# Kernel optimization log

Measured on AMD Instinct MI355X. Metric: run time of the kernel, lower is better.

The kernel has to match this reference:

```python
import jax, jax.numpy as jnp
import numpy as np

N = 100000
E = 1600000
IN_C = 64
HID_C = 64
OUT_C = 64
GW = 0.8
EPS = 1e-5


def setup_inputs() -> dict:
    key = jax.random.key(0)
    ks = jax.random.split(key, 8)
    node_features = jax.random.normal(ks[0], (N, IN_C), dtype=jnp.float32)
    edges = jax.random.randint(ks[1], (2, E), 0, N, dtype=jnp.int64)
    s1 = 1.0 / np.sqrt(IN_C)
    s2 = 1.0 / np.sqrt(HID_C)
    W1 = jax.random.uniform(ks[2], (IN_C, HID_C), jnp.float32, -s1, s1)
    b1 = jnp.zeros((HID_C,), jnp.float32)
    W2 = jax.random.uniform(ks[3], (HID_C, OUT_C), jnp.float32, -s2, s2)
    b2 = jnp.zeros((OUT_C,), jnp.float32)
    ln_w = jnp.ones((1,), jnp.float32)
    ln_b = jnp.zeros((1,), jnp.float32)
    return {"node_features": node_features, "edges": edges, "W1": W1, "b1": b1,
            "W2": W2, "b2": b2, "ln_w": ln_w, "ln_b": ln_b}


def _gcn_conv(x, W, b, src, dst, enorm, n):
    # GCNConv: D^{-1/2}(A+I)D^{-1/2} X W + b  (self-loops already in src/dst)
    xw = x @ W                              # [N, F]
    msg = xw[src] * enorm[:, None]          # gather + scale, [E+N, F]
    out = jax.ops.segment_sum(msg, dst, num_segments=n)
    return out + b


def reference(node_features, edges, W1, b1, W2, b2, ln_w, ln_b):
    n = node_features.shape[0]
    loops = jnp.arange(n, dtype=edges.dtype)
    src = jnp.concatenate([edges[0], loops])
    dst = jnp.concatenate([edges[1], loops])
    deg = jax.ops.segment_sum(jnp.ones_like(dst, dtype=node_features.dtype), dst, num_segments=n)
    dis = jnp.where(deg > 0, jax.lax.rsqrt(deg), 0.0)
    enorm = dis[src] * dis[dst]

    # both branches apply the same conv1 to the same input (dropout off in eval)
    h = jax.nn.relu(_gcn_conv(node_features, W1, b1, src, dst, enorm, n))
    x = GW * h + (1.0 - GW) * h
    x = jax.nn.relu(_gcn_conv(x, W2, b2, src, dst, enorm, n))
    # PyG LayerNorm, mode='graph', batch=None: normalize over all nodes+channels
    mean = jnp.mean(x)
    var = jnp.mean((x - mean) ** 2)
    x = (x - mean) * jax.lax.rsqrt(var + EPS) * ln_w + ln_b
    return x
```

## Files before the change

### kernel.cpp

```cpp
#include <hip/hip_runtime.h>
#include <hip/hip_bf16.h>

#define CH 64
#define BSH 9
#define CHUNK 16384
#define MAXB 10240


__global__ __launch_bounds__(1024)
void coarse_hist_kernel(const int* __restrict__ dst, int* __restrict__ blockHist,
                        int E, int nb) {
    __shared__ int h[256];
    int t = threadIdx.x;
    for (int i = t; i < nb; i += 1024) h[i] = 0;
    __syncthreads();
    int base = blockIdx.x * CHUNK + t * 16;
#pragma unroll
    for (int j = 0; j < 16; j += 4) {
        int e = base + j;
        if (e + 3 < E) {
            int4 d = *(const int4*)(dst + e);
            atomicAdd(&h[d.x >> BSH], 1);
            atomicAdd(&h[d.y >> BSH], 1);
            atomicAdd(&h[d.z >> BSH], 1);
            atomicAdd(&h[d.w >> BSH], 1);
        } else {
            for (int k = e; k < E && k < e + 4; ++k) atomicAdd(&h[dst[k] >> BSH], 1);
        }
    }
    __syncthreads();
    for (int i = t; i < nb; i += 1024) blockHist[blockIdx.x * nb + i] = h[i];
}

__global__ __launch_bounds__(256)
void scan_hist_kernel(int* __restrict__ blockHist, int* __restrict__ bucketStart,
                      int nblk, int nb) {
    __shared__ int tots[256];
    __shared__ int scn[257];
    int t = threadIdx.x;
    if (t < nb) {
        int s = 0;
        for (int blk = 0; blk < nblk; ++blk) s += blockHist[blk * nb + t];
        tots[t] = s;
    }
    __syncthreads();
    if (t == 0) {
        int r = 0;
        for (int b = 0; b < nb; ++b) { scn[b] = r; r += tots[b]; }
        scn[nb] = r;
    }
    __syncthreads();
    if (t < nb) {
        int r = scn[t];
        for (int blk = 0; blk < nblk; ++blk) {
            int v = blockHist[blk * nb + t];
            blockHist[blk * nb + t] = r;
            r += v;
        }
    }
    if (t <= nb) bucketStart[t] = scn[t];
}

__global__ __launch_bounds__(1024)
void scatter_pairs_kernel(const int* __restrict__ src, const int* __restrict__ dst,
                          const int* __restrict__ blockBase, unsigned* __restrict__ pairs,
                          int E, int nb) {
    __shared__ int cur[256];
    int t = threadIdx.x;
    for (int i = t; i < nb; i += 1024) cur[i] = blockBase[blockIdx.x * nb + i];
    __syncthreads();
    int base = blockIdx.x * CHUNK + t * 16;
#pragma unroll
    for (int j = 0; j < 16; j += 4) {
        int e = base + j;
        if (e + 3 < E) {
            int4 d = *(const int4*)(dst + e);
            int4 s = *(const int4*)(src + e);
            int p0 = atomicAdd(&cur[d.x >> BSH], 1);
            pairs[p0] = ((unsigned)(d.x & 511) << 17) | (unsigned)s.x;
            int p1 = atomicAdd(&cur[d.y >> BSH], 1);
            pairs[p1] = ((unsigned)(d.y & 511) << 17) | (unsigned)s.y;
            int p2 = atomicAdd(&cur[d.z >> BSH], 1);
            pairs[p2] = ((unsigned)(d.z & 511) << 17) | (unsigned)s.z;
            int p3 = atomicAdd(&cur[d.w >> BSH], 1);
            pairs[p3] = ((unsigned)(d.w & 511) << 17) | (unsigned)s.w;
        } else {
            for (int k = e; k < E && k < e + 4; ++k) {
                int d = dst[k];
                int p = atomicAdd(&cur[d >> BSH], 1);
                pairs[p] = ((unsigned)(d & 511) << 17) | (unsigned)src[k];
            }
        }
    }
}

__global__ __launch_bounds__(1024)
void bucket_csr_kernel(const unsigned* __restrict__ pairs, const int* __restrict__ bucketStart,
                       int* __restrict__ col, int* __restrict__ rs, float* __restrict__ dis,
                       int N, int nb) {
    __shared__ int hist[512];
    __shared__ int offs[512];
    __shared__ int cursor[512];
    __shared__ int lcol[MAXB];
    int b = blockIdx.x;
    int t = threadIdx.x;
    int n0 = b << BSH;
    int nn = min(512, N - n0);
    int start = bucketStart[b];
    int endp = bucketStart[b + 1];
    int cnt = endp - start;
    bool big = cnt > MAXB;
    for (int i = t; i < nn; i += 1024) hist[i] = 0;
    __syncthreads();
    for (int i = start + t; i < endp; i += 1024) {
        unsigned p = pairs[i];
        atomicAdd(&hist[p >> 17], 1);
    }
    __syncthreads();
    if (t < 512) offs[t] = (t < nn) ? hist[t] : 0;
    __syncthreads();
    for (int off = 1; off < 512; off <<= 1) {
        int a = (t < 512 && t >= off) ? offs[t - off] : 0;
        __syncthreads();
        if (t < 512) offs[t] += a;
        __syncthreads();
    }
    if (t < nn) {
        int excl = offs[t] - hist[t];
        rs[n0 + t] = start + excl;
        dis[n0 + t] = rsqrtf((float)hist[t] + 1.0f);
        cursor[t] = excl;
    }
    __syncthreads();
    for (int i = start + t; i < endp; i += 1024) {
        unsigned p = pairs[i];
        int pos = atomicAdd(&cursor[p >> 17], 1);
        int sv = (int)(p & 0x1FFFFu);
        if (big) col[start + pos] = sv;
        else lcol[pos] = sv;
    }
    __syncthreads();
    if (!big) {
        for (int i = t; i < cnt; i += 1024) col[start + i] = lcol[i];
    }
}


__device__ inline unsigned pack_bf2(float a, float b) {
    __hip_bfloat162 t;
    t.x = __float2bfloat16(a);
    t.y = __float2bfloat16(b);
    unsigned u;
    __builtin_memcpy(&u, &t, 4);
    return u;
}

__device__ inline float bf_lo(unsigned u) {
    unsigned w = u << 16; float f; __builtin_memcpy(&f, &w, 4); return f;
}
__device__ inline float bf_hi(unsigned u) {
    unsigned w = u & 0xffff0000u; float f; __builtin_memcpy(&f, &w, 4); return f;
}

__device__ inline unsigned ldu(const unsigned* p, unsigned boff) {
    return *(const unsigned*)((const char*)p + boff);
}

#define FMA16(xs0, xs1, wa, wb)                                              \
    a00 += (xs0) * (wa).x; a01 += (xs0) * (wa).y;                            \
    a02 += (xs0) * (wa).z; a03 += (xs0) * (wa).w;                            \
    a04 += (xs0) * (wb).x; a05 += (xs0) * (wb).y;                            \
    a06 += (xs0) * (wb).z; a07 += (xs0) * (wb).w;                            \
    a10 += (xs1) * (wa).x; a11 += (xs1) * (wa).y;                            \
    a12 += (xs1) * (wa).z; a13 += (xs1) * (wa).w;                            \
    a14 += (xs1) * (wb).x; a15 += (xs1) * (wb).y;                            \
    a16 += (xs1) * (wb).z; a17 += (xs1) * (wb).w;

__global__ __launch_bounds__(256, 4)
void gemm64_scaled_kernel(const float* __restrict__ X, const float* __restrict__ W,
                          const float* __restrict__ dis,
                          __hip_bfloat16* __restrict__ Y, int n) {
    __shared__ float Ws[CH * CH];
    {
        float4* w4 = (float4*)Ws;
        const float4* g4 = (const float4*)W;
        for (int i = threadIdx.x; i < CH * CH / 4; i += 256) w4[i] = g4[i];
    }
    __syncthreads();
    int t = threadIdx.x;
    int cbase = (t & 7) * 8;
    int r0 = blockIdx.x * 64 + (t >> 3) * 2;
    if (r0 >= n) return;
    int r1c = min(r0 + 1, n - 1);
    const float4* p0 = (const float4*)(X + (size_t)r0 * CH);
    const float4* p1 = (const float4*)(X + (size_t)r1c * CH);

    float a00 = 0.f, a01 = 0.f, a02 = 0.f, a03 = 0.f;
    float a04 = 0.f, a05 = 0.f, a06 = 0.f, a07 = 0.f;
    float a10 = 0.f, a11 = 0.f, a12 = 0.f, a13 = 0.f;
    float a14 = 0.f, a15 = 0.f, a16 = 0.f, a17 = 0.f;

#pragma unroll 4
    for (int k4 = 0; k4 < CH / 4; ++k4) {
        float4 xa = p0[k4];
        float4 xb = p1[k4];
        const float* wr = &Ws[(k4 * 4) * CH + cbase];
        float4 wa, wb;
        wa = *(const float4*)(wr);
        wb = *(const float4*)(wr + 4);
        FMA16(xa.x, xb.x, wa, wb)
        wa = *(const float4*)(wr + CH);
        wb = *(const float4*)(wr + CH + 4);
        FMA16(xa.y, xb.y, wa, wb)
        wa = *(const float4*)(wr + 2 * CH);
        wb = *(const float4*)(wr + 2 * CH + 4);
        FMA16(xa.z, xb.z, wa, wb)
        wa = *(const float4*)(wr + 3 * CH);
        wb = *(const float4*)(wr + 3 * CH + 4);
        FMA16(xa.w, xb.w, wa, wb)
    }

    float d0 = dis[r0];
    uint4 pk;
    pk.x = pack_bf2(a00 * d0, a01 * d0);
    pk.y = pack_bf2(a02 * d0, a03 * d0);
    pk.z = pack_bf2(a04 * d0, a05 * d0);
    pk.w = pack_bf2(a06 * d0, a07 * d0);
    *(uint4*)(Y + (size_t)r0 * CH + cbase) = pk;
    if (r0 + 1 < n) {
        float d1 = dis[r0 + 1];
        pk.x = pack_bf2(a10 * d1, a11 * d1);
        pk.y = pack_bf2(a12 * d1, a13 * d1);
        pk.z = pack_bf2(a14 * d1, a15 * d1);
        pk.w = pack_bf2(a16 * d1, a17 * d1);
        *(uint4*)(Y + (size_t)(r0 + 1) * CH + cbase) = pk;
    }
}

#define GATHER_SHFL_BODY(XWS)                                                 \
    int beg = rs[wid];                                                        \
    int end = (wid + 1 < n) ? rs[wid + 1] : E;                                \
    unsigned cp4 = (unsigned)cp << 2;                                         \
    float accx = 0.f, accy = 0.f;                                             \
    for (int base = beg; base < end; base += 64) {                            \
        int cnt = min(64, end - base);                                        \
        int myCol = (base + lane < end) ? col[base + lane] : 0;               \
        int eb = 0;                                                           \
        for (; eb + 16 <= cnt; eb += 16) {                                    \
            unsigned o0 = ((unsigned)__shfl(myCol, eb + half, 64) << 7) | cp4;      \
            unsigned o1 = ((unsigned)__shfl(myCol, eb + 2 + half, 64) << 7) | cp4;  \
            unsigned o2 = ((unsigned)__shfl(myCol, eb + 4 + half, 64) << 7) | cp4;  \
            unsigned o3 = ((unsigned)__shfl(myCol, eb + 6 + half, 64) << 7) | cp4;  \
            unsigned o4 = ((unsigned)__shfl(myCol, eb + 8 + half, 64) << 7) | cp4;  \
            unsigned o5 = ((unsigned)__shfl(myCol, eb + 10 + half, 64) << 7) | cp4; \
            unsigned o6 = ((unsigned)__shfl(myCol, eb + 12 + half, 64) << 7) | cp4; \
            unsigned o7 = ((unsigned)__shfl(myCol, eb + 14 + half, 64) << 7) | cp4; \
            unsigned u0 = ldu((XWS), o0);                                     \
            unsigned u1 = ldu((XWS), o1);                                     \
            unsigned u2 = ldu((XWS), o2);                                     \
            unsigned u3 = ldu((XWS), o3);                                     \
            unsigned u4 = ldu((XWS), o4);                                     \
            unsigned u5 = ldu((XWS), o5);                                     \
            unsigned u6 = ldu((XWS), o6);                                     \
            unsigned u7 = ldu((XWS), o7);                                     \
            accx += bf_lo(u0) + bf_lo(u1) + bf_lo(u2) + bf_lo(u3);            \
            accy += bf_hi(u0) + bf_hi(u1) + bf_hi(u2) + bf_hi(u3);            \
            accx += bf_lo(u4) + bf_lo(u5) + bf_lo(u6) + bf_lo(u7);            \
            accy += bf_hi(u4) + bf_hi(u5) + bf_hi(u6) + bf_hi(u7);            \
        }                                                                     \
        for (; eb + 8 <= cnt; eb += 8) {                                      \
            unsigned o0 = ((unsigned)__shfl(myCol, eb + half, 64) << 7) | cp4;      \
            unsigned o1 = ((unsigned)__shfl(myCol, eb + 2 + half, 64) << 7) | cp4;  \
            unsigned o2 = ((unsigned)__shfl(myCol, eb + 4 + half, 64) << 7) | cp4;  \
            unsigned o3 = ((unsigned)__shfl(myCol, eb + 6 + half, 64) << 7) | cp4;  \
            unsigned u0 = ldu((XWS), o0);                                     \
            unsigned u1 = ldu((XWS), o1);                                     \
            unsigned u2 = ldu((XWS), o2);                                     \
            unsigned u3 = ldu((XWS), o3);                                     \
            accx += bf_lo(u0) + bf_lo(u1) + bf_lo(u2) + bf_lo(u3);            \
            accy += bf_hi(u0) + bf_hi(u1) + bf_hi(u2) + bf_hi(u3);            \
        }                                                                     \
        for (; eb + 1 < cnt; eb += 2) {                                       \
            unsigned o = ((unsigned)__shfl(myCol, eb + half, 64) << 7) | cp4; \
            unsigned u = ldu((XWS), o);                                       \
            accx += bf_lo(u); accy += bf_hi(u);                               \
        }                                                                     \
        if (eb < cnt) { \
            unsigned o = ((unsigned)__shfl(myCol, eb, 64) << 7) | cp4;        \
            unsigned u = ldu((XWS), o);                                       \
            if (half == 0) { accx += bf_lo(u); accy += bf_hi(u); }            \
        }                                                                     \
    }                                                                         \
    accx += __shfl_xor(accx, 32, 64);                                         \
    accy += __shfl_xor(accy, 32, 64);

__global__ __launch_bounds__(256)
void gather_pair_kernel(const unsigned* __restrict__ xws, const int* __restrict__ col,
                        const int* __restrict__ rs, const float* __restrict__ dis,
                        const float* __restrict__ b1, float* __restrict__ h,
                        int n, int E) {
    int wid = blockIdx.x * 4 + (threadIdx.x >> 6);
    int lane = threadIdx.x & 63;
    int cp = lane & 31;
    int half = lane >> 5;
    if (wid >= n) return;

    GATHER_SHFL_BODY(xws)

    if (half == 0) {
        float dd = dis[wid];
        unsigned us = xws[(size_t)wid * 32 + cp];
        float2 bb = ((const float2*)b1)[cp];
        float2 o;
        o.x = fmaxf(dd * (accx + bf_lo(us)) + bb.x, 0.f);
        o.y = fmaxf(dd * (accy + bf_hi(us)) + bb.y, 0.f);
        ((float2*)h)[(size_t)wid * 32 + cp] = o;
    }
}

__global__ __launch_bounds__(256)
void gather_stats_kernel(const unsigned* __restrict__ xws, const int* __restrict__ col,
                         const int* __restrict__ rs, const float* __restrict__ dis,
                         const float* __restrict__ b2, float* __restrict__ out,
                         int n, int E, float* __restrict__ sums, float* __restrict__ sqs) {
    int wid = blockIdx.x * 4 + (threadIdx.x >> 6);
    int lane = threadIdx.x & 63;
    int cp = lane & 31;
    int half = lane >> 5;
    float vx = 0.f, vy = 0.f;
    if (wid < n) {
        GATHER_SHFL_BODY(xws)
        float dd = dis[wid];
        unsigned us = xws[(size_t)wid * 32 + cp];
        float2 bb = ((const float2*)b2)[cp];
        vx = fmaxf(dd * (accx + bf_lo(us)) + bb.x, 0.f);
        vy = fmaxf(dd * (accy + bf_hi(us)) + bb.y, 0.f);
        if (half == 0) {
            float2 o; o.x = vx; o.y = vy;
            ((float2*)out)[(size_t)wid * 32 + cp] = o;
        }
    }
    float s = (half == 0) ? vx + vy : 0.f;
    float sq = (half == 0) ? vx * vx + vy * vy : 0.f;
#pragma unroll
    for (int off = 32; off > 0; off >>= 1) {
        s += __shfl_down(s, off, 64);
        sq += __shfl_down(sq, off, 64);
    }
    __shared__ float ls[4], lq[4];
    int w = threadIdx.x >> 6;
    if ((threadIdx.x & 63) == 0) { ls[w] = s; lq[w] = sq; }
    __syncthreads();
    if (threadIdx.x == 0) {
        sums[blockIdx.x] = ls[0] + ls[1] + ls[2] + ls[3];
        sqs[blockIdx.x] = lq[0] + lq[1] + lq[2] + lq[3];
    }
}

__global__ void reduce_final_kernel(const float* __restrict__ sums, const float* __restrict__ sqs,
                                    int nb, float n_total, const float* __restrict__ lnw,
                                    const float* __restrict__ lnb, float* __restrict__ so) {
    float s = 0.0f, sq = 0.0f;
    for (int i = threadIdx.x; i < nb; i += 1024) { s += sums[i]; sq += sqs[i]; }
#pragma unroll
    for (int off = 32; off > 0; off >>= 1) {
        s += __shfl_down(s, off, 64);
        sq += __shfl_down(sq, off, 64);
    }
    __shared__ float ls[16], lq[16];
    int w = threadIdx.x >> 6;
    if ((threadIdx.x & 63) == 0) { ls[w] = s; lq[w] = sq; }
    __syncthreads();
    if (threadIdx.x == 0) {
        float ts = 0.0f, tq = 0.0f;
        for (int i = 0; i < 16; ++i) { ts += ls[i]; tq += lq[i]; }
        float mean = ts / n_total;
        float var = tq / n_total - mean * mean;
        float scale = rsqrtf(var + 1e-5f) * lnw[0];
        so[0] = scale;
        so[1] = lnb[0] - mean * scale;
    }
}

__global__ void norm_kernel(float* __restrict__ x, int n4, const float* __restrict__ so) {
    int i = blockIdx.x * blockDim.x + threadIdx.x;
    if (i >= n4) return;
    float scale = so[0], off = so[1];
    float4* x4 = (float4*)x;
    float4 v = x4[i];
    v.x = v.x * scale + off;
    v.y = v.y * scale + off;
    v.z = v.z * scale + off;
    v.w = v.w * scale + off;
    x4[i] = v;
}

extern "C" void kernel_launch(void* const* d_in, const int* in_sizes, int n_in,
                              void* d_out, int out_size, void* d_ws, size_t ws_size,
                              hipStream_t stream) {
    const float* X   = (const float*)d_in[0];
    const int*   edg = (const int*)d_in[1];
    const float* W1  = (const float*)d_in[2];
    const float* b1  = (const float*)d_in[3];
    const float* W2  = (const float*)d_in[4];
    const float* b2  = (const float*)d_in[5];
    const float* lnw = (const float*)d_in[6];
    const float* lnb = (const float*)d_in[7];
    float* out = (float*)d_out;

    const int N  = in_sizes[0] / CH;
    const int E  = in_sizes[1] / 2;
    const int NC = N * CH;
    const int nNodeBlk = (N + 3) / 4;
    const int nb = (N + 511) >> BSH;
    const int nblkE = (E + CHUNK - 1) / CHUNK;

    const int* srcp = edg;
    const int* dstp = edg + E;

    int*   col   = (int*)d_ws;
    int*   rs    = col + E;
    float* dis   = (float*)(rs + N);
    __hip_bfloat16* xws1 = (__hip_bfloat16*)(dis + N);
    __hip_bfloat16* xws2 = xws1 + NC;
    float* h     = (float*)(xws2 + NC);
    unsigned* pairs = (unsigned*)h;
    int*   bHist = (int*)(h + NC);
    int*   bStart= bHist + nblkE * nb;
    float* sums  = (float*)(bStart + nb + 1);
    float* sqs   = sums + nNodeBlk;
    float* so    = sqs + nNodeBlk;

    const int B = 256;
    const int nGemmBlk = (N + 63) / 64;

    coarse_hist_kernel<<<nblkE, 1024, 0, stream>>>(dstp, bHist, E, nb);
    scan_hist_kernel<<<1, 256, 0, stream>>>(bHist, bStart, nblkE, nb);
    scatter_pairs_kernel<<<nblkE, 1024, 0, stream>>>(srcp, dstp, bHist, pairs, E, nb);
    bucket_csr_kernel<<<nb, 1024, 0, stream>>>(pairs, bStart, col, rs, dis, N, nb);

    gemm64_scaled_kernel<<<nGemmBlk, B, 0, stream>>>(X, W1, dis, xws1, N);
    gather_pair_kernel<<<nNodeBlk, B, 0, stream>>>((const unsigned*)xws1, col, rs, dis,
                                                   b1, h, N, E);

    gemm64_scaled_kernel<<<nGemmBlk, B, 0, stream>>>(h, W2, dis, xws2, N);
    gather_stats_kernel<<<nNodeBlk, B, 0, stream>>>((const unsigned*)xws2, col, rs, dis,
                                                    b2, out, N, E, sums, sqs);

    reduce_final_kernel<<<1, 1024, 0, stream>>>(sums, sqs, nNodeBlk, (float)NC, lnw, lnb, so);
    norm_kernel<<<(NC / 4 + B - 1) / B, B, 0, stream>>>(out, NC / 4, so);
}
```

Measured before the change: 297.6 us.

## Widen gather loads to 16B per lane, 4-row GEMM tiles, atomic LayerNorm stats

The gather kernels now have each lane load 16 bytes (8 bf16 channels), so eight lanes cover one 128-byte row and eight edges are gathered in parallel per wave, followed by a cross-group shuffle reduction. This replaces the earlier 4-byte-per-lane scheme. The GEMM computes four rows per thread instead of two, which improves weight reuse from shared memory but raises register pressure. The per-block stats plus separate reduce kernel are replaced by global float atomics into two scalars, with mean and variance folded into the norm kernel. That removes one launch but makes the summation order nondeterministic.

Result: slower. 567.1 us (+90.6%).

```diff
diff --git a/kernel.cpp b/kernel.cpp
--- a/kernel.cpp
+++ b/kernel.cpp
@@ -34,10 +34,11 @@
 
 __global__ __launch_bounds__(256)
 void scan_hist_kernel(int* __restrict__ blockHist, int* __restrict__ bucketStart,
-                      int nblk, int nb) {
+                      int nblk, int nb, float* __restrict__ so) {
     __shared__ int tots[256];
     __shared__ int scn[257];
     int t = threadIdx.x;
+    if (t == 0) { so[2] = 0.f; so[3] = 0.f; }
     if (t < nb) {
         int s = 0;
         for (int blk = 0; blk < nblk; ++blk) s += blockHist[blk * nb + t];
@@ -162,19 +163,27 @@
     unsigned w = u & 0xffff0000u; float f; __builtin_memcpy(&f, &w, 4); return f;
 }
 
-__device__ inline unsigned ldu(const unsigned* p, unsigned boff) {
-    return *(const unsigned*)((const char*)p + boff);
-}
-
-#define FMA16(xs0, xs1, wa, wb)                                              \
-    a00 += (xs0) * (wa).x; a01 += (xs0) * (wa).y;                            \
-    a02 += (xs0) * (wa).z; a03 += (xs0) * (wa).w;                            \
-    a04 += (xs0) * (wb).x; a05 += (xs0) * (wb).y;                            \
-    a06 += (xs0) * (wb).z; a07 += (xs0) * (wb).w;                            \
-    a10 += (xs1) * (wa).x; a11 += (xs1) * (wa).y;                            \
-    a12 += (xs1) * (wa).z; a13 += (xs1) * (wa).w;                            \
-    a14 += (xs1) * (wb).x; a15 += (xs1) * (wb).y;                            \
-    a16 += (xs1) * (wb).z; a17 += (xs1) * (wb).w;
+__device__ inline uint4 ldx4(const unsigned* p, unsigned boff) {
+    return *(const uint4*)((const char*)p + boff);
+}
+
+#define FMA32(x0, x1, x2, x3, wa, wb)                                        \
+    a00 += (x0) * (wa).x; a01 += (x0) * (wa).y;                              \
+    a02 += (x0) * (wa).z; a03 += (x0) * (wa).w;                              \
+    a04 += (x0) * (wb).x; a05 += (x0) * (wb).y;                              \
+    a06 += (x0) * (wb).z; a07 += (x0) * (wb).w;                              \
+    a10 += (x1) * (wa).x; a11 += (x1) * (wa).y;                              \
+    a12 += (x1) * (wa).z; a13 += (x1) * (wa).w;                              \
+    a14 += (x1) * (wb).x; a15 += (x1) * (wb).y;                              \
+    a16 += (x1) * (wb).z; a17 += (x1) * (wb).w;                              \
+    a20 += (x2) * (wa).x; a21 += (x2) * (wa).y;                              \
+    a22 += (x2) * (wa).z; a23 += (x2) * (wa).w;                              \
+    a24 += (x2) * (wb).x; a25 += (x2) * (wb).y;                              \
+    a26 += (x2) * (wb).z; a27 += (x2) * (wb).w;                              \
+    a30 += (x3) * (wa).x; a31 += (x3) * (wa).y;                              \
+    a32 += (x3) * (wa).z; a33 += (x3) * (wa).w;                              \
+    a34 += (x3) * (wb).x; a35 += (x3) * (wb).y;                              \
+    a36 += (x3) * (wb).z; a37 += (x3) * (wb).w;
 
 __global__ __launch_bounds__(256, 4)
 void gemm64_scaled_kernel(const float* __restrict__ X, const float* __restrict__ W,
@@ -189,39 +198,49 @@
     __syncthreads();
     int t = threadIdx.x;
     int cbase = (t & 7) * 8;
-    int r0 = blockIdx.x * 64 + (t >> 3) * 2;
+    int r0 = blockIdx.x * 128 + (t >> 3) * 4;
     if (r0 >= n) return;
-    int r1c = min(r0 + 1, n - 1);
-    const float4* p0 = (const float4*)(X + (size_t)r0 * CH);
-    const float4* p1 = (const float4*)(X + (size_t)r1c * CH);
+    int rB = min(r0 + 1, n - 1);
+    int rC = min(r0 + 2, n - 1);
+    int rD = min(r0 + 3, n - 1);
+    const float4* pA = (const float4*)(X + (size_t)r0 * CH);
+    const float4* pB = (const float4*)(X + (size_t)rB * CH);
+    const float4* pC = (const float4*)(X + (size_t)rC * CH);
+    const float4* pD = (const float4*)(X + (size_t)rD * CH);
 
     float a00 = 0.f, a01 = 0.f, a02 = 0.f, a03 = 0.f;
     float a04 = 0.f, a05 = 0.f, a06 = 0.f, a07 = 0.f;
     float a10 = 0.f, a11 = 0.f, a12 = 0.f, a13 = 0.f;
     float a14 = 0.f, a15 = 0.f, a16 = 0.f, a17 = 0.f;
-
-#pragma unroll 4
+    float a20 = 0.f, a21 = 0.f, a22 = 0.f, a23 = 0.f;
+    float a24 = 0.f, a25 = 0.f, a26 = 0.f, a27 = 0.f;
+    float a30 = 0.f, a31 = 0.f, a32 = 0.f, a33 = 0.f;
+    float a34 = 0.f, a35 = 0.f, a36 = 0.f, a37 = 0.f;
+
+#pragma unroll 2
     for (int k4 = 0; k4 < CH / 4; ++k4) {
-        float4 xa = p0[k4];
-        float4 xb = p1[k4];
+        float4 xa = pA[k4];
+        float4 xb = pB[k4];
+        float4 xc = pC[k4];
+        float4 xd = pD[k4];
         const float* wr = &Ws[(k4 * 4) * CH + cbase];
         float4 wa, wb;
         wa = *(const float4*)(wr);
         wb = *(const float4*)(wr + 4);
-        FMA16(xa.x, xb.x, wa, wb)
+        FMA32(xa.x, xb.x, xc.x, xd.x, wa, wb)
         wa = *(const float4*)(wr + CH);
         wb = *(const float4*)(wr + CH + 4);
-        FMA16(xa.y, xb.y, wa, wb)
+        FMA32(xa.y, xb.y, xc.y, xd.y, wa, wb)
         wa = *(const float4*)(wr + 2 * CH);
         wb = *(const float4*)(wr + 2 * CH + 4);
-        FMA16(xa.z, xb.z, wa, wb)
+        FMA32(xa.z, xb.z, xc.z, xd.z, wa, wb)
         wa = *(const float4*)(wr + 3 * CH);
         wb = *(const float4*)(wr + 3 * CH + 4);
-        FMA16(xa.w, xb.w, wa, wb)
-    }
-
+        FMA32(xa.w, xb.w, xc.w, xd.w, wa, wb)
+    }
+
+    uint4 pk;
     float d0 = dis[r0];
-    uint4 pk;
     pk.x = pack_bf2(a00 * d0, a01 * d0);
     pk.y = pack_bf2(a02 * d0, a03 * d0);
     pk.z = pack_bf2(a04 * d0, a05 * d0);
@@ -235,64 +254,72 @@
         pk.w = pack_bf2(a16 * d1, a17 * d1);
         *(uint4*)(Y + (size_t)(r0 + 1) * CH + cbase) = pk;
     }
-}
-
-#define GATHER_SHFL_BODY(XWS)                                                 \
+    if (r0 + 2 < n) {
+        float d2 = dis[r0 + 2];
+        pk.x = pack_bf2(a20 * d2, a21 * d2);
+        pk.y = pack_bf2(a22 * d2, a23 * d2);
+        pk.z = pack_bf2(a24 * d2, a25 * d2);
+        pk.w = pack_bf2(a26 * d2, a27 * d2);
+        *(uint4*)(Y + (size_t)(r0 + 2) * CH + cbase) = pk;
+    }
+    if (r0 + 3 < n) {
+        float d3 = dis[r0 + 3];
+        pk.x = pack_bf2(a30 * d3, a31 * d3);
+        pk.y = pack_bf2(a32 * d3, a33 * d3);
+        pk.z = pack_bf2(a34 * d3, a35 * d3);
+        pk.w = pack_bf2(a36 * d3, a37 * d3);
+        *(uint4*)(Y + (size_t)(r0 + 3) * CH + cbase) = pk;
+    }
+}
+
+#define ACC8(u)                                                               \
+    aL0 += bf_lo((u).x); aH0 += bf_hi((u).x);                                 \
+    aL1 += bf_lo((u).y); aH1 += bf_hi((u).y);                                 \
+    aL2 += bf_lo((u).z); aH2 += bf_hi((u).z);                                 \
+    aL3 += bf_lo((u).w); aH3 += bf_hi((u).w);
+
+#define RED3(v)                                                               \
+    v += __shfl_xor(v, 8, 64);                                                \
+    v += __shfl_xor(v, 16, 64);                                               \
+    v += __shfl_xor(v, 32, 64);
+
+#define GATHER_X4_BODY(XWS)                                                   \
     int beg = rs[wid];                                                        \
     int end = (wid + 1 < n) ? rs[wid + 1] : E;                                \
-    unsigned cp4 = (unsigned)cp << 2;                                         \
-    float accx = 0.f, accy = 0.f;                                             \
+    unsigned sub16 = (unsigned)(lane & 7) << 4;                               \
+    int grp = lane >> 3;                                                      \
+    float aL0 = 0.f, aH0 = 0.f, aL1 = 0.f, aH1 = 0.f;                         \
+    float aL2 = 0.f, aH2 = 0.f, aL3 = 0.f, aH3 = 0.f;                         \
+    uint4 uself = ldx4((XWS), ((unsigned)wid << 7) | sub16);     \
+    float dd = dis[wid];                                                      \
     for (int base = beg; base < end; base += 64) {                            \
         int cnt = min(64, end - base);                                        \
         int myCol = (base + lane < end) ? col[base + lane] : 0;               \
         int eb = 0;                                                           \
         for (; eb + 16 <= cnt; eb += 16) {                                    \
-            unsigned o0 = ((unsigned)__shfl(myCol, eb + half, 64) << 7) | cp4;      \
-            unsigned o1 = ((unsigned)__shfl(myCol, eb + 2 + half, 64) << 7) | cp4;  \
-            unsigned o2 = ((unsigned)__shfl(myCol, eb + 4 + half, 64) << 7) | cp4;  \
-            unsigned o3 = ((unsigned)__shfl(myCol, eb + 6 + half, 64) << 7) | cp4;  \
-            unsigned o4 = ((unsigned)__shfl(myCol, eb + 8 + half, 64) << 7) | cp4;  \
-            unsigned o5 = ((unsigned)__shfl(myCol, eb + 10 + half, 64) << 7) | cp4; \
-            unsigned o6 = ((unsigned)__shfl(myCol, eb + 12 + half, 64) << 7) | cp4; \
-            unsigned o7 = ((unsigned)__shfl(myCol, eb + 14 + half, 64) << 7) | cp4; \
-            unsigned u0 = ldu((XWS), o0);                                     \
-            unsigned u1 = ldu((XWS), o1);                                     \
-            unsigned u2 = ldu((XWS), o2);                                     \
-            unsigned u3 = ldu((XWS), o3);                                     \
-            unsigned u4 = ldu((XWS), o4);                                     \
-            unsigned u5 = ldu((XWS), o5);                                     \
-            unsigned u6 = ldu((XWS), o6);                                     \
-            unsigned u7 = ldu((XWS), o7);                                     \
-            accx += bf_lo(u0) + bf_lo(u1) + bf_lo(u2) + bf_lo(u3);            \
-            accy += bf_hi(u0) + bf_hi(u1) + bf_hi(u2) + bf_hi(u3);            \
-            accx += bf_lo(u4) + bf_lo(u5) + bf_lo(u6) + bf_lo(u7);            \
-            accy += bf_hi(u4) + bf_hi(u5) + bf_hi(u6) + bf_hi(u7);            \
+            unsigned o0 = ((unsigned)__shfl(myCol, eb + grp, 64) << 7) | sub16;     \
+            unsigned o1 = ((unsigned)__shfl(myCol, eb + 8 + grp, 64) << 7) | sub16; \
+            uint4 u0 = ldx4((XWS), o0);                                       \
+            uint4 u1 = ldx4((XWS), o1);                                       \
+            ACC8(u0)                                                          \
+            ACC8(u1)                                                          \
         }                                                                     \
-        for (; eb + 8 <= cnt; eb += 8) {                                      \
-            unsigned o0 = ((unsigned)__shfl(myCol, eb + half, 64) << 7) | cp4;      \
-            unsigned o1 = ((unsigned)__shfl(myCol, eb + 2 + half, 64) << 7) | cp4;  \
-            unsigned o2 = ((unsigned)__shfl(myCol, eb + 4 + half, 64) << 7) | cp4;  \
-            unsigned o3 = ((unsigned)__shfl(myCol, eb + 6 + half, 64) << 7) | cp4;  \
-            unsigned u0 = ldu((XWS), o0);                                     \
-            unsigned u1 = ldu((XWS), o1);                                     \
-            unsigned u2 = ldu((XWS), o2);                                     \
-            unsigned u3 = ldu((XWS), o3);                                     \
-            accx += bf_lo(u0) + bf_lo(u1) + bf_lo(u2) + bf_lo(u3);            \
-            accy += bf_hi(u0) + bf_hi(u1) + bf_hi(u2) + bf_hi(u3);            \
-        }                                                                     \
-        for (; eb + 1 < cnt; eb += 2) {                                       \
-            unsigned o = ((unsigned)__shfl(myCol, eb + half, 64) << 7) | cp4; \
-            unsigned u = ldu((XWS), o);                                       \
-            accx += bf_lo(u); accy += bf_hi(u);                               \
-        }                                                                     \
-        if (eb < cnt) { \
-            unsigned o = ((unsigned)__shfl(myCol, eb, 64) << 7) | cp4;        \
-            unsigned u = ldu((XWS), o);                                       \
-            if (half == 0) { accx += bf_lo(u); accy += bf_hi(u); }            \
+        for (; eb < cnt; eb += 8) {                                           \
+            int ei = eb + grp;                                                \
+            int ec = ei < cnt ? ei : cnt - 1;                                 \
+            unsigned o = ((unsigned)__shfl(myCol, ec, 64) << 7) | sub16;      \
+            uint4 u = ldx4((XWS), o);                                         \
+            if (ei < cnt) { ACC8(u) }                                         \
         }                                                                     \
     }                                                                         \
-    accx += __shfl_xor(accx, 32, 64);                                         \
-    accy += __shfl_xor(accy, 32, 64);
+    if (grp == 0) { ACC8(uself) }    \
+    RED3(aL0) RED3(aH0) RED3(aL1) RED3(aH1)                                   \
+    RED3(aL2) RED3(aH2) RED3(aL3) RED3(aH3)                                   \
+    int g01 = grp & 1;                                                        \
+    float t0 = g01 ? aL2 : aL0;                                               \
+    float t1 = g01 ? aH2 : aH0;                                               \
+    float t2 = g01 ? aL3 : aL1;                                               \
+    float t3 = g01 ? aH3 : aH1;
 
 __global__ __launch_bounds__(256)
 void gather_pair_kernel(const unsigned* __restrict__ xws, const int* __restrict__ col,
@@ -301,47 +328,42 @@
                         int n, int E) {
     int wid = blockIdx.x * 4 + (threadIdx.x >> 6);
     int lane = threadIdx.x & 63;
-    int cp = lane & 31;
-    int half = lane >> 5;
     if (wid >= n) return;
 
-    GATHER_SHFL_BODY(xws)
-
-    if (half == 0) {
-        float dd = dis[wid];
-        unsigned us = xws[(size_t)wid * 32 + cp];
-        float2 bb = ((const float2*)b1)[cp];
-        float2 o;
-        o.x = fmaxf(dd * (accx + bf_lo(us)) + bb.x, 0.f);
-        o.y = fmaxf(dd * (accy + bf_hi(us)) + bb.y, 0.f);
-        ((float2*)h)[(size_t)wid * 32 + cp] = o;
-    }
+    GATHER_X4_BODY(xws)
+
+    float4 bb = ((const float4*)b1)[((lane & 7) << 1) | g01];
+    float4 o;
+    o.x = fmaxf(dd * t0 + bb.x, 0.f);
+    o.y = fmaxf(dd * t1 + bb.y, 0.f);
+    o.z = fmaxf(dd * t2 + bb.z, 0.f);
+    o.w = fmaxf(dd * t3 + bb.w, 0.f);
+    if (grp < 2)
+        ((float4*)h)[(size_t)wid * 16 + ((lane & 7) << 1) + g01] = o;
 }
 
 __global__ __launch_bounds__(256)
 void gather_stats_kernel(const unsigned* __restrict__ xws, const int* __restrict__ col,
                          const int* __restrict__ rs, const float* __restrict__ dis,
                          const float* __restrict__ b2, float* __restrict__ out,
-                         int n, int E, float* __restrict__ sums, float* __restrict__ sqs) {
+                         int n, int E, float* __restrict__ so) {
     int wid = blockIdx.x * 4 + (threadIdx.x >> 6);
     int lane = threadIdx.x & 63;
-    int cp = lane & 31;
-    int half = lane >> 5;
-    float vx = 0.f, vy = 0.f;
+    float s = 0.f, sq = 0.f;
     if (wid < n) {
-        GATHER_SHFL_BODY(xws)
-        float dd = dis[wid];
-        unsigned us = xws[(size_t)wid * 32 + cp];
-        float2 bb = ((const float2*)b2)[cp];
-        vx = fmaxf(dd * (accx + bf_lo(us)) + bb.x, 0.f);
-        vy = fmaxf(dd * (accy + bf_hi(us)) + bb.y, 0.f);
-        if (half == 0) {
-            float2 o; o.x = vx; o.y = vy;
-            ((float2*)out)[(size_t)wid * 32 + cp] = o;
+        GATHER_X4_BODY(xws)
+        float4 bb = ((const float4*)b2)[((lane & 7) << 1) | g01];
+        float4 o;
+        o.x = fmaxf(dd * t0 + bb.x, 0.f);
+        o.y = fmaxf(dd * t1 + bb.y, 0.f);
+        o.z = fmaxf(dd * t2 + bb.z, 0.f);
+        o.w = fmaxf(dd * t3 + bb.w, 0.f);
+        if (grp < 2) {
+            ((float4*)out)[(size_t)wid * 16 + ((lane & 7) << 1) + g01] = o;
+            s = o.x + o.y + o.z + o.w;
+            sq = o.x * o.x + o.y * o.y + o.z * o.z + o.w * o.w;
         }
     }
-    float s = (half == 0) ? vx + vy : 0.f;
-    float sq = (half == 0) ? vx * vx + vy * vy : 0.f;
 #pragma unroll
     for (int off = 32; off > 0; off >>= 1) {
         s += __shfl_down(s, off, 64);
@@ -352,40 +374,20 @@
     if ((threadIdx.x & 63) == 0) { ls[w] = s; lq[w] = sq; }
     __syncthreads();
     if (threadIdx.x == 0) {
-        sums[blockIdx.x] = ls[0] + ls[1] + ls[2] + ls[3];
-        sqs[blockIdx.x] = lq[0] + lq[1] + lq[2] + lq[3];
-    }
-}
-
-__global__ void reduce_final_kernel(const float* __restrict__ sums, const float* __restrict__ sqs,
-                                    int nb, float n_total, const float* __restrict__ lnw,
-                                    const float* __restrict__ lnb, float* __restrict__ so) {
-    float s = 0.0f, sq = 0.0f;
-    for (int i = threadIdx.x; i < nb; i += 1024) { s += sums[i]; sq += sqs[i]; }
-#pragma unroll
-    for (int off = 32; off > 0; off >>= 1) {
-        s += __shfl_down(s, off, 64);
-        sq += __shfl_down(sq, off, 64);
-    }
-    __shared__ float ls[16], lq[16];
-    int w = threadIdx.x >> 6;
-    if ((threadIdx.x & 63) == 0) { ls[w] = s; lq[w] = sq; }
-    __syncthreads();
-    if (threadIdx.x == 0) {
-        float ts = 0.0f, tq = 0.0f;
-        for (int i = 0; i < 16; ++i) { ts += ls[i]; tq += lq[i]; }
-        float mean = ts / n_total;
-        float var = tq / n_total - mean * mean;
-        float scale = rsqrtf(var + 1e-5f) * lnw[0];
-        so[0] = scale;
-        so[1] = lnb[0] - mean * scale;
-    }
-}
-
-__global__ void norm_kernel(float* __restrict__ x, int n4, const float* __restrict__ so) {
+        atomicAdd(&so[2], ls[0] + ls[1] + ls[2] + ls[3]);
+        atomicAdd(&so[3], lq[0] + lq[1] + lq[2] + lq[3]);
+    }
+}
+
+__global__ void norm_kernel(float* __restrict__ x, int n4, const float* __restrict__ so,
+                            float inv_n, const float* __restrict__ lnw,
+                            const float* __restrict__ lnb) {
     int i = blockIdx.x * blockDim.x + threadIdx.x;
     if (i >= n4) return;
-    float scale = so[0], off = so[1];
+    float mean = so[2] * inv_n;
+    float var = so[3] * inv_n - mean * mean;
+    float scale = rsqrtf(var + 1e-5f) * lnw[0];
+    float off = lnb[0] - mean * scale;
     float4* x4 = (float4*)x;
     float4 v = x4[i];
     v.x = v.x * scale + off;
@@ -427,15 +429,13 @@
     unsigned* pairs = (unsigned*)h;
     int*   bHist = (int*)(h + NC);
     int*   bStart= bHist + nblkE * nb;
-    float* sums  = (float*)(bStart + nb + 1);
-    float* sqs   = sums + nNodeBlk;
-    float* so    = sqs + nNodeBlk;
+    float* so    = (float*)(bStart + nb + 1);
 
     const int B = 256;
-    const int nGemmBlk = (N + 63) / 64;
+    const int nGemmBlk = (N + 127) / 128;
 
     coarse_hist_kernel<<<nblkE, 1024, 0, stream>>>(dstp, bHist, E, nb);
-    scan_hist_kernel<<<1, 256, 0, stream>>>(bHist, bStart, nblkE, nb);
+    scan_hist_kernel<<<1, 256, 0, stream>>>(bHist, bStart, nblkE, nb, so);
     scatter_pairs_kernel<<<nblkE, 1024, 0, stream>>>(srcp, dstp, bHist, pairs, E, nb);
     bucket_csr_kernel<<<nb, 1024, 0, stream>>>(pairs, bStart, col, rs, dis, N, nb);
 
@@ -445,8 +445,7 @@
 
     gemm64_scaled_kernel<<<nGemmBlk, B, 0, stream>>>(h, W2, dis, xws2, N);
     gather_stats_kernel<<<nNodeBlk, B, 0, stream>>>((const unsigned*)xws2, col, rs, dis,
-                                                    b2, out, N, E, sums, sqs);
-
-    reduce_final_kernel<<<1, 1024, 0, stream>>>(sums, sqs, nNodeBlk, (float)NC, lnw, lnb, so);
-    norm_kernel<<<(NC / 4 + B - 1) / B, B, 0, stream>>>(out, NC / 4, so);
-}
+                                                    b2, out, N, E, so);
+
+    norm_kernel<<<(NC / 4 + B - 1) / B, B, 0, stream>>>(out, NC / 4, so, 1.0f / NC, lnw, lnb);
+}
```
